# Optimization experiments

Measured on AMD Instinct MI355X. Metric: run time of the kernel, lower is better.

Reference implementation:

```python
import jax, jax.numpy as jnp
import numpy as np

B, L, E, H = 8, 2048, 256, 4
D = E // H  # head_dim = 64


def setup_inputs() -> dict:
    key = jax.random.key(0)
    k1, k2, k3, k4, k5 = jax.random.split(key, 5)
    x = jax.random.normal(k1, (B, L, E), dtype=jnp.float32)
    # torch.nn.MultiheadAttention packed in-projection: weight [3E, E], bias [3E]
    lim = float(np.sqrt(6.0 / (3 * E + E)))  # xavier_uniform on [3E, E]
    in_proj_w = jax.random.uniform(k2, (3 * E, E), dtype=jnp.float32, minval=-lim, maxval=lim)
    in_proj_b = jnp.zeros((3 * E,), dtype=jnp.float32)
    # W_gnn: xavier_uniform on [E, E]; B_gnn: randn [E]
    limw = float(np.sqrt(6.0 / (E + E)))
    W_gnn = jax.random.uniform(k3, (E, E), dtype=jnp.float32, minval=-limw, maxval=limw)
    B_gnn = jax.random.normal(k4, (E,), dtype=jnp.float32)
    return {"x": x, "in_proj_w": in_proj_w, "in_proj_b": in_proj_b,
            "W_gnn": W_gnn, "B_gnn": B_gnn}


def reference(x, in_proj_w, in_proj_b, W_gnn, B_gnn):
    # --- MultiheadAttention(x, x, x), batch_first=True, need_weights=True ---
    qkv = x @ in_proj_w.T + in_proj_b                      # [B, L, 3E]
    q, k, v = jnp.split(qkv, 3, axis=-1)                   # each [B, L, E]
    # split heads -> [B, H, L, D]
    q = q.reshape(B, L, H, D).transpose(0, 2, 1, 3)
    k = k.reshape(B, L, H, D).transpose(0, 2, 1, 3)
    scale = 1.0 / jnp.sqrt(jnp.float32(D))
    scores = jnp.einsum('bhqd,bhkd->bhqk', q * scale, k)   # [B, H, L, L]
    attn = jax.nn.softmax(scores, axis=-1)
    # need_weights=True (average_attn_weights default True): head-averaged probs
    b = attn.mean(axis=1)                                  # [B, L, L]
    # NOTE: MHA output `a` (out_proj(attn @ v)) is discarded by the module,
    # so out_proj / value path do not affect the result.
    # --- x = bmm(b, x) @ W_gnn + B_gnn ---
    agg = jnp.einsum('bql,bld->bqd', b, x)                 # [B, L, E]
    return agg @ W_gnn + B_gnn
```

## Files before the change

kernel.cpp:

```cpp
#include <hip/hip_runtime.h>

#define B_ 8
#define L_ 2048
#define E_ 256
#define H_ 4
#define D_ 64

typedef __bf16 bf16;
typedef __bf16 bf16x8 __attribute__((ext_vector_type(8)));
typedef __bf16 bf16x4 __attribute__((ext_vector_type(4)));
typedef float  f32x4  __attribute__((ext_vector_type(4)));
typedef float  f32x16 __attribute__((ext_vector_type(16)));

#define QSCALE 0.1803368801111244f

__device__ __forceinline__ float fexp2(float x) { return __builtin_amdgcn_exp2f(x); }
__device__ __forceinline__ float flog2(float x) { return __builtin_amdgcn_logf(x); }

__device__ __forceinline__ void barrier_lds() {
    asm volatile("s_waitcnt lgkmcnt(0)" ::: "memory");
    __builtin_amdgcn_s_barrier();
}

__global__ void prep_kernel(const float* __restrict__ x,
                            const float* __restrict__ in_proj_w,
                            const float* __restrict__ W_gnn,
                            bf16* __restrict__ xb, bf16* __restrict__ Wcat) {
    int bid = blockIdx.x;
    if (bid < 4096) {
        size_t i = ((size_t)bid * 256 + threadIdx.x) * 4;
        f32x4 v = *(const f32x4*)&x[i];
        bf16x4 o;
#pragma unroll
        for (int j = 0; j < 4; j++) o[j] = (bf16)v[j];
        *(bf16x4*)&xb[i] = o;
    } else {
        int r = bid - 4096;
        int e = threadIdx.x;
        float v = (r < 512) ? in_proj_w[r * E_ + e] : W_gnn[e * E_ + (r - 512)];
        Wcat[r * E_ + e] = (bf16)v;
    }
}

__global__ __launch_bounds__(256, 2) void proj_kernel(
    const bf16* __restrict__ xb, const bf16* __restrict__ Wcat,
    const float* __restrict__ in_proj_b, const float* __restrict__ B_gnn,
    bf16* __restrict__ Qs, bf16* __restrict__ Ks, bf16* __restrict__ XWT) {
    __shared__ bf16 ldsW[2][256 * 36];
    int tid  = threadIdx.x;
    int lane = tid & 63, wave = tid >> 6;
    int l16  = lane & 15, quad = lane >> 4;
    int m0 = blockIdx.x * 64 + wave * 16;
    int by = blockIdx.y;
    int n0 = by * 256;

    f32x4 acc[16];
#pragma unroll
    for (int i = 0; i < 16; i++) acc[i] = (f32x4){0.f, 0.f, 0.f, 0.f};

    bf16x8 af[8];
    const bf16* xrow = xb + (size_t)(m0 + l16) * E_;
#pragma unroll
    for (int ks = 0; ks < 8; ks++) af[ks] = *(const bf16x8*)&xrow[ks * 32 + quad * 8];

    const bf16* Wb = Wcat + (size_t)n0 * E_;

#pragma unroll
    for (int it = 0; it < 4; it++) {
        int idx = it * 256 + tid;
        int n = idx >> 2, c8 = (idx & 3) * 8;
        *(bf16x8*)&ldsW[0][n * 36 + c8] = *(const bf16x8*)&Wb[(size_t)n * E_ + c8];
    }
    __syncthreads();

    int cur = 0;
    for (int ks = 0; ks < 8; ks++) {
        bf16x8 pw[4];
        if (ks < 7) {
#pragma unroll
            for (int it = 0; it < 4; it++) {
                int idx = it * 256 + tid;
                int n = idx >> 2, c8 = (idx & 3) * 8;
                pw[it] = *(const bf16x8*)&Wb[(size_t)n * E_ + (ks + 1) * 32 + c8];
            }
        }
#pragma unroll
        for (int nt = 0; nt < 16; nt++) {
            bf16x8 bfv = *(const bf16x8*)&ldsW[cur][(nt * 16 + l16) * 36 + quad * 8];
            acc[nt] = __builtin_amdgcn_mfma_f32_16x16x32_bf16(af[ks], bfv, acc[nt], 0, 0, 0);
        }
        if (ks < 7) {
#pragma unroll
            for (int it = 0; it < 4; it++) {
                int idx = it * 256 + tid;
                int n = idx >> 2, c8 = (idx & 3) * 8;
                *(bf16x8*)&ldsW[cur ^ 1][n * 36 + c8] = pw[it];
            }
        }
        barrier_lds();
        cur ^= 1;
    }

#pragma unroll
    for (int nt = 0; nt < 16; nt++) {
        int n = n0 + nt * 16 + l16;
        if (by == 0) {
            float bias = in_proj_b[n];
#pragma unroll
            for (int r = 0; r < 4; r++) {
                int m = m0 + quad * 4 + r;
                Qs[(size_t)m * E_ + n] = (bf16)((acc[nt][r] + bias) * QSCALE);
            }
        } else if (by == 1) {
            float bias = in_proj_b[n];
            int col = n - 256;
#pragma unroll
            for (int r = 0; r < 4; r++) {
                int m = m0 + quad * 4 + r;
                Ks[(size_t)m * E_ + col] = (bf16)(acc[nt][r] + bias);
            }
        } else {
            int nc = n - 512;
            float bias = B_gnn[nc];
            int m = m0 + quad * 4;
            int b = m >> 11, l = m & 2047;
            bf16x4 pk;
#pragma unroll
            for (int r = 0; r < 4; r++) pk[r] = (bf16)(acc[nt][r] + bias);
            *(bf16x4*)&XWT[((size_t)b * E_ + nc) * L_ + l] = pk;
        }
    }
}

__global__ __launch_bounds__(256, 4) void stats_kernel(
    const bf16* __restrict__ Qs, const bf16* __restrict__ Ks,
    float* __restrict__ o) {
    __shared__ bf16 ldsK[2][128 * 72];
    int tid  = threadIdx.x;
    int lane = tid & 63, wave = tid >> 6;
    int r32  = lane & 31, half = lane >> 5;
    int qt = blockIdx.x, h = blockIdx.y, b = blockIdx.z;
    int q0 = qt * 128 + wave * 32;

    bf16x8 qa[4];
    const bf16* qrow = Qs + ((size_t)b * L_ + q0 + r32) * E_ + h * D_;
#pragma unroll
    for (int c = 0; c < 4; c++) qa[c] = *(const bf16x8*)&qrow[c * 16 + half * 8];

    float lsum[16];
#pragma unroll
    for (int i = 0; i < 16; i++) lsum[i] = 0.f;

    const bf16* Kb = Ks + (size_t)b * L_ * E_ + h * D_;

#pragma unroll
    for (int it = 0; it < 4; it++) {
        int idx = it * 256 + tid;
        int key = idx >> 3, dc = (idx & 7) * 8;
        *(bf16x8*)&ldsK[0][key * 72 + dc] =
            *(const bf16x8*)&Kb[(size_t)key * E_ + dc];
    }
    __syncthreads();

    int cur = 0;
    for (int kt = 0; kt < 16; kt++) {
        bf16x8 pk[4];
        if (kt < 15) {
#pragma unroll
            for (int it = 0; it < 4; it++) {
                int idx = it * 256 + tid;
                pk[it] = *(const bf16x8*)&Kb[(size_t)((kt + 1) * 128 + (idx >> 3)) * E_ + (idx & 7) * 8];
            }
        }
#pragma unroll
        for (int nt = 0; nt < 4; nt++) {
            f32x16 S = {};
#pragma unroll
            for (int c = 0; c < 4; c++) {
                bf16x8 kb = *(const bf16x8*)&ldsK[cur][(nt * 32 + r32) * 72 + c * 16 + half * 8];
                S = __builtin_amdgcn_mfma_f32_32x32x16_bf16(qa[c], kb, S, 0, 0, 0);
            }
#pragma unroll
            for (int i = 0; i < 16; i++) lsum[i] += fexp2(S[i]);
        }
        if (kt < 15) {
#pragma unroll
            for (int it = 0; it < 4; it++) {
                int idx = it * 256 + tid;
                *(bf16x8*)&ldsK[cur ^ 1][(idx >> 3) * 72 + (idx & 7) * 8] = pk[it];
            }
        }
        barrier_lds();
        cur ^= 1;
    }
#pragma unroll
    for (int i = 0; i < 16; i++) {
        float v = lsum[i];
        v += __shfl_xor(v, 1); v += __shfl_xor(v, 2); v += __shfl_xor(v, 4);
        v += __shfl_xor(v, 8); v += __shfl_xor(v, 16);
        lsum[i] = v;
    }
    if (r32 == 0) {
        float* op = o + ((size_t)(b * H_ + h)) * L_ + q0;
#pragma unroll
        for (int i = 0; i < 16; i++) {
            int row = (i & 3) + 8 * (i >> 2) + 4 * half;
            op[row] = -(2.0f + flog2(lsum[i]));
        }
    }
}

__global__ void __launch_bounds__(512) __attribute__((amdgpu_waves_per_eu(2, 2)))
pass2_kernel(
    const bf16* __restrict__ Qs, const bf16* __restrict__ Ks,
    const bf16* __restrict__ XWT, const float* __restrict__ o,
    float* __restrict__ out) {
    __shared__ alignas(16) unsigned char smem[159744];
    bf16* ldsK0  = (bf16*)smem;
    bf16* ldsK1  = (bf16*)(smem + 33792);
    bf16* ldsXW0 = (bf16*)(smem + 67584);
    bf16* ldsXW1 = (bf16*)(smem + 104448);
    bf16* ldsP0  = (bf16*)(smem + 141312);
    bf16* ldsP1  = (bf16*)(smem + 150528);

    int tid  = threadIdx.x;
    int lane = tid & 63, wave = tid >> 6;
    int l32  = lane & 31, half = lane >> 5;

    int flat = blockIdx.x;
    int b  = flat & 7;
    int qt = flat >> 3;
    int q0 = qt * 64;

    const bf16* Kb = Ks + (size_t)b * L_ * E_;
    const bf16* Xb = XWT + (size_t)b * E_ * L_;

#pragma unroll
    for (int it = 0; it < 4; it++) {
        int idx = it * 512 + tid;
        int key = idx >> 5, col = (idx & 31) * 8;
        *(bf16x8*)&ldsK0[key * 264 + col] =
            *(const bf16x8*)&Kb[(size_t)key * E_ + col];
    }
    __syncthreads();

    if (wave < 4) {
        int pqh = wave & 1, pkh = wave >> 1;
        int qw = q0 + pqh * 32 + l32;

        bf16x8 qf[4][4];
        const bf16* qrow = Qs + ((size_t)b * L_ + qw) * E_;
#pragma unroll
        for (int h = 0; h < H_; h++)
#pragma unroll
            for (int c = 0; c < 4; c++)
                qf[h][c] = *(const bf16x8*)&qrow[h * 64 + c * 16 + half * 8];

        float oh[4];
#pragma unroll
        for (int h = 0; h < H_; h++)
            oh[h] = o[((size_t)(b * H_ + h)) * L_ + qw];

        f32x16 zero = {};
        for (int kt = 0; kt < 32; kt++) {
            bf16* kcur = (kt & 1) ? ldsK1  : ldsK0;
            bf16* xcur = (kt & 1) ? ldsXW1 : ldsXW0;
            bf16* pcur = (kt & 1) ? ldsP1  : ldsP0;

            bf16x8 pxf[8];
#pragma unroll
            for (int it = 0; it < 8; it++) {
                int idx = it * 256 + tid;
                int n = idx >> 3, kc8 = (idx & 7) * 8;
                pxf[it] = *(const bf16x8*)&Xb[(size_t)n * L_ + kt * 64 + kc8];
            }

            f32x16 P = zero;
#pragma unroll
            for (int h = 0; h < H_; h++) {
                f32x16 s = zero;
#pragma unroll
                for (int c = 0; c < 4; c++) {
                    bf16x8 ka = *(const bf16x8*)&kcur[(pkh * 32 + l32) * 264 + h * 64 + c * 16 + half * 8];
                    s = __builtin_amdgcn_mfma_f32_32x32x16_bf16(ka, qf[h][c], s, 0, 0, 0);
                }
#pragma unroll
                for (int r = 0; r < 16; r++) P[r] += fexp2(s[r] + oh[h]);
            }

#pragma unroll
            for (int g = 0; g < 4; g++) {
                bf16x4 pk;
#pragma unroll
                for (int j = 0; j < 4; j++) pk[j] = (bf16)P[4 * g + j];
                *(bf16x4*)&pcur[(pqh * 32 + l32) * 72 + pkh * 32 + g * 8 + half * 4] = pk;
            }

#pragma unroll
            for (int it = 0; it < 8; it++) {
                int idx = it * 256 + tid;
                int n = idx >> 3, kc8 = (idx & 7) * 8;
                *(bf16x8*)&xcur[n * 72 + kc8] = pxf[it];
            }
            barrier_lds();
        }
    } else {
        int cw = wave - 4;
        int cqh = cw & 1, cnh = cw >> 1;
        int ctid = tid - 256;

        f32x16 zero = {};
        f32x16 acc[4];
#pragma unroll
        for (int i = 0; i < 4; i++) acc[i] = zero;

        for (int kt = 0; kt < 32; kt++) {
            bf16* knext = (kt & 1) ? ldsK0  : ldsK1;
            bf16* xprev = (kt & 1) ? ldsXW0 : ldsXW1;
            bf16* pprev = (kt & 1) ? ldsP0  : ldsP1;

            bf16x8 pkf[8];
            if (kt < 31) {
#pragma unroll
                for (int it = 0; it < 8; it++) {
                    int idx = it * 256 + ctid;
                    int key = idx >> 5, col = (idx & 31) * 8;
                    pkf[it] = *(const bf16x8*)&Kb[(size_t)((kt + 1) * 64 + key) * E_ + col];
                }
            }

            if (kt > 0) {
#pragma unroll
                for (int kc = 0; kc < 4; kc++) {
                    bf16x8 pa = *(const bf16x8*)&pprev[(cqh * 32 + l32) * 72 + kc * 16 + half * 8];
#pragma unroll
                    for (int nt = 0; nt < 4; nt++) {
                        bf16x8 xw = *(const bf16x8*)&xprev[(cnh * 128 + nt * 32 + l32) * 72 + kc * 16 + half * 8];
                        acc[nt] = __builtin_amdgcn_mfma_f32_32x32x16_bf16(pa, xw, acc[nt], 0, 0, 0);
                    }
                }
            }

            if (kt < 31) {
#pragma unroll
                for (int it = 0; it < 8; it++) {
                    int idx = it * 256 + ctid;
                    int key = idx >> 5, col = (idx & 31) * 8;
                    *(bf16x8*)&knext[key * 264 + col] = pkf[it];
                }
            }
            barrier_lds();
        }

#pragma unroll
        for (int kc = 0; kc < 4; kc++) {
            bf16x8 pa = *(const bf16x8*)&ldsP1[(cqh * 32 + l32) * 72 + kc * 16 + half * 8];
#pragma unroll
            for (int nt = 0; nt < 4; nt++) {
                bf16x8 xw = *(const bf16x8*)&ldsXW1[(cnh * 128 + nt * 32 + l32) * 72 + kc * 16 + half * 8];
                acc[nt] = __builtin_amdgcn_mfma_f32_32x32x16_bf16(pa, xw, acc[nt], 0, 0, 0);
            }
        }

        float* Ob = out + ((size_t)b * L_ + q0 + cqh * 32) * E_ + cnh * 128;
#pragma unroll
        for (int nt = 0; nt < 4; nt++)
#pragma unroll
            for (int r = 0; r < 16; r++) {
                int row = (r & 3) + 8 * (r >> 2) + 4 * half;
                Ob[(size_t)row * E_ + nt * 32 + l32] = acc[nt][r];
            }
    }
}

extern "C" void kernel_launch(void* const* d_in, const int* in_sizes, int n_in,
                              void* d_out, int out_size, void* d_ws, size_t ws_size,
                              hipStream_t stream) {
    const float* x   = (const float*)d_in[0];
    const float* ipw = (const float*)d_in[1];
    const float* ipb = (const float*)d_in[2];
    const float* wg  = (const float*)d_in[3];
    const float* bg  = (const float*)d_in[4];

    char* ws = (char*)d_ws;
    bf16*  Qs   = (bf16*)(ws);
    bf16*  Ks   = (bf16*)(ws + 8388608);
    bf16*  XWT  = (bf16*)(ws + 16777216);
    float* o    = (float*)(ws + 25165824);
    bf16*  xb   = (bf16*)(ws + 25427968);
    bf16*  Wcat = (bf16*)(ws + 33816576);

    prep_kernel<<<4864, 256, 0, stream>>>(x, ipw, wg, xb, Wcat);
    proj_kernel<<<dim3(256, 3), 256, 0, stream>>>(xb, Wcat, ipb, bg, Qs, Ks, XWT);
    stats_kernel<<<dim3(16, 4, 8), 256, 0, stream>>>(Qs, Ks, o);
    pass2_kernel<<<256, 512, 0, stream>>>(Qs, Ks, XWT, o, (float*)d_out);
}
```

Before: 174.7 us.

## Fuse x bf16 conversion into projection, remap grids batch-fastest, fold offset into MFMA init

The separate fp32-to-bf16 conversion of x is removed, and the projection kernel now reads fp32 x directly and converts it in registers, avoiding a full write and reread of the bf16 copy. The projection and stats kernels switch to flat 1D grids whose block index varies the batch fastest, which changes the order blocks are scheduled in and how they share cache. In pass2 the per-head log-sum offset is loaded into the MFMA accumulator at the start, so the add is gone from the exp loop. The projection now reads twice as many bytes of x per block, and that read is repeated across the three output column groups.

New measurement: 179.1 us. +2.5%, slower.

```diff
diff --git a/kernel.cpp b/kernel.cpp
--- a/kernel.cpp
+++ b/kernel.cpp
@@ -22,46 +22,47 @@
     __builtin_amdgcn_s_barrier();
 }
 
-__global__ void prep_kernel(const float* __restrict__ x,
-                            const float* __restrict__ in_proj_w,
+__global__ void prep_kernel(const float* __restrict__ in_proj_w,
                             const float* __restrict__ W_gnn,
-                            bf16* __restrict__ xb, bf16* __restrict__ Wcat) {
-    int bid = blockIdx.x;
-    if (bid < 4096) {
-        size_t i = ((size_t)bid * 256 + threadIdx.x) * 4;
-        f32x4 v = *(const f32x4*)&x[i];
-        bf16x4 o;
-#pragma unroll
-        for (int j = 0; j < 4; j++) o[j] = (bf16)v[j];
-        *(bf16x4*)&xb[i] = o;
-    } else {
-        int r = bid - 4096;
-        int e = threadIdx.x;
-        float v = (r < 512) ? in_proj_w[r * E_ + e] : W_gnn[e * E_ + (r - 512)];
-        Wcat[r * E_ + e] = (bf16)v;
-    }
+                            bf16* __restrict__ Wcat) {
+    int r = blockIdx.x;
+    int e = threadIdx.x;
+    float v = (r < 512) ? in_proj_w[r * E_ + e] : W_gnn[e * E_ + (r - 512)];
+    Wcat[r * E_ + e] = (bf16)v;
 }
 
 __global__ __launch_bounds__(256, 2) void proj_kernel(
-    const bf16* __restrict__ xb, const bf16* __restrict__ Wcat,
+    const float* __restrict__ x, const bf16* __restrict__ Wcat,
     const float* __restrict__ in_proj_b, const float* __restrict__ B_gnn,
     bf16* __restrict__ Qs, bf16* __restrict__ Ks, bf16* __restrict__ XWT) {
     __shared__ bf16 ldsW[2][256 * 36];
     int tid  = threadIdx.x;
     int lane = tid & 63, wave = tid >> 6;
     int l16  = lane & 15, quad = lane >> 4;
-    int m0 = blockIdx.x * 64 + wave * 16;
-    int by = blockIdx.y;
-    int n0 = by * 256;
+
+    int flat = blockIdx.x;
+    int b   = flat & 7;
+    int s   = flat >> 3;
+    int by  = s >> 5;
+    int mtl = s & 31;
+    int m0  = b * 2048 + mtl * 64 + wave * 16;
+    int n0  = by * 256;
 
     f32x4 acc[16];
 #pragma unroll
     for (int i = 0; i < 16; i++) acc[i] = (f32x4){0.f, 0.f, 0.f, 0.f};
 
     bf16x8 af[8];
-    const bf16* xrow = xb + (size_t)(m0 + l16) * E_;
-#pragma unroll
-    for (int ks = 0; ks < 8; ks++) af[ks] = *(const bf16x8*)&xrow[ks * 32 + quad * 8];
+    const float* xrow = x + (size_t)(m0 + l16) * E_;
+#pragma unroll
+    for (int ks = 0; ks < 8; ks++) {
+        f32x4 lo = *(const f32x4*)&xrow[ks * 32 + quad * 8];
+        f32x4 hi = *(const f32x4*)&xrow[ks * 32 + quad * 8 + 4];
+        bf16x8 v;
+#pragma unroll
+        for (int j = 0; j < 4; j++) { v[j] = (bf16)lo[j]; v[4 + j] = (bf16)hi[j]; }
+        af[ks] = v;
+    }
 
     const bf16* Wb = Wcat + (size_t)n0 * E_;
 
@@ -123,11 +124,11 @@
             int nc = n - 512;
             float bias = B_gnn[nc];
             int m = m0 + quad * 4;
-            int b = m >> 11, l = m & 2047;
+            int bb = m >> 11, l = m & 2047;
             bf16x4 pk;
 #pragma unroll
             for (int r = 0; r < 4; r++) pk[r] = (bf16)(acc[nt][r] + bias);
-            *(bf16x4*)&XWT[((size_t)b * E_ + nc) * L_ + l] = pk;
+            *(bf16x4*)&XWT[((size_t)bb * E_ + nc) * L_ + l] = pk;
         }
     }
 }
@@ -139,7 +140,12 @@
     int tid  = threadIdx.x;
     int lane = tid & 63, wave = tid >> 6;
     int r32  = lane & 31, half = lane >> 5;
-    int qt = blockIdx.x, h = blockIdx.y, b = blockIdx.z;
+
+    int flat = blockIdx.x;
+    int b    = flat & 7;
+    int rest = flat >> 3;
+    int qt   = rest & 15;
+    int h    = rest >> 4;
     int q0 = qt * 128 + wave * 32;
 
     bf16x8 qa[4];
@@ -261,7 +267,6 @@
         for (int h = 0; h < H_; h++)
             oh[h] = o[((size_t)(b * H_ + h)) * L_ + qw];
 
-        f32x16 zero = {};
         for (int kt = 0; kt < 32; kt++) {
             bf16* kcur = (kt & 1) ? ldsK1  : ldsK0;
             bf16* xcur = (kt & 1) ? ldsXW1 : ldsXW0;
@@ -275,17 +280,19 @@
                 pxf[it] = *(const bf16x8*)&Xb[(size_t)n * L_ + kt * 64 + kc8];
             }
 
-            f32x16 P = zero;
+            f32x16 P = {};
 #pragma unroll
             for (int h = 0; h < H_; h++) {
-                f32x16 s = zero;
+                f32x16 s;
+#pragma unroll
+                for (int r = 0; r < 16; r++) s[r] = oh[h];
 #pragma unroll
                 for (int c = 0; c < 4; c++) {
                     bf16x8 ka = *(const bf16x8*)&kcur[(pkh * 32 + l32) * 264 + h * 64 + c * 16 + half * 8];
                     s = __builtin_amdgcn_mfma_f32_32x32x16_bf16(ka, qf[h][c], s, 0, 0, 0);
                 }
 #pragma unroll
-                for (int r = 0; r < 16; r++) P[r] += fexp2(s[r] + oh[h]);
+                for (int r = 0; r < 16; r++) P[r] += fexp2(s[r]);
             }
 
 #pragma unroll
@@ -387,11 +394,10 @@
     bf16*  Ks   = (bf16*)(ws + 8388608);
     bf16*  XWT  = (bf16*)(ws + 16777216);
     float* o    = (float*)(ws + 25165824);
-    bf16*  xb   = (bf16*)(ws + 25427968);
     bf16*  Wcat = (bf16*)(ws + 33816576);
 
-    prep_kernel<<<4864, 256, 0, stream>>>(x, ipw, wg, xb, Wcat);
-    proj_kernel<<<dim3(256, 3), 256, 0, stream>>>(xb, Wcat, ipb, bg, Qs, Ks, XWT);
-    stats_kernel<<<dim3(16, 4, 8), 256, 0, stream>>>(Qs, Ks, o);
+    prep_kernel<<<768, 256, 0, stream>>>(ipw, wg, Wcat);
+    proj_kernel<<<768, 256, 0, stream>>>(x, Wcat, ipb, bg, Qs, Ks, XWT);
+    stats_kernel<<<512, 256, 0, stream>>>(Qs, Ks, o);
     pass2_kernel<<<256, 512, 0, stream>>>(Qs, Ks, XWT, o, (float*)d_out);
 }
```
